# Optimization experiments

Hardware: AMD Instinct MI355X
Metric: run time of the kernel (lower is better)

The kernel has to match this reference:

```python
import jax, jax.numpy as jnp
import numpy as np

N = 50000        # nodes
E = 800000       # edges
F_IN = 128       # dataset.num_features (== dim*heads so all conv layers share in_channels)
DIM = 32         # mParams['dim']
HEADS = 4        # mParams['num_heads']
HC = DIM * HEADS # 128
DEPTH = 2        # mParams['c_depth'] -> total conv layers = DEPTH + 1 = 3
L = DEPTH + 1
DIM2 = 16        # ceil(DIM/2)
NCLS = 6
SLOPE = 0.2      # GATv2Conv default negative_slope


def setup_inputs() -> dict:
    key = jax.random.key(0)
    ks = jax.random.split(key, 20)
    def lin(k, fan_in, shape):
        return jax.random.normal(k, shape, dtype=jnp.float32) / np.sqrt(fan_in)
    x = jax.random.normal(ks[0], (N, F_IN), dtype=jnp.float32)
    edge_index = jax.random.randint(ks[1], (2, E), 0, N, dtype=jnp.int64)
    batch = jnp.zeros((N,), dtype=jnp.int64)
    # stacked GATv2Conv params (all layers have in_channels = 128)
    Wl = lin(ks[2], F_IN, (L, F_IN, HC))   # lin_l weight (source transform)
    Wr = lin(ks[3], F_IN, (L, F_IN, HC))   # lin_r weight (target transform)
    bl = jnp.zeros((L, HC), dtype=jnp.float32)
    br = jnp.zeros((L, HC), dtype=jnp.float32)
    att = lin(ks[4], DIM, (L, HEADS, DIM)) # attention vector a
    cb = jnp.zeros((L, HC), dtype=jnp.float32)  # conv output bias
    W1 = lin(ks[5], HC, (HC, DIM));   b1 = jnp.zeros((DIM,), jnp.float32)
    W2 = lin(ks[6], DIM, (DIM, DIM2)); b2 = jnp.zeros((DIM2,), jnp.float32)
    W3 = lin(ks[7], 2 * DIM2, (2 * DIM2, NCLS)); b3 = jnp.zeros((NCLS,), jnp.float32)
    return {"x": x, "edge_index": edge_index, "batch": batch,
            "Wl": Wl, "Wr": Wr, "bl": bl, "br": br, "att": att, "cb": cb,
            "W1": W1, "b1": b1, "W2": W2, "b2": b2, "W3": W3, "b3": b3}


def _gatv2_layer(h, src, dst, Wl, Wr, bl, br, att, cb):
    # h: [N, F]; src/dst: [Ea] (self-loops included)
    xl = (h @ Wl + bl).reshape(N, HEADS, DIM)  # source-side transform
    xr = (h @ Wr + br).reshape(N, HEADS, DIM)  # target-side transform
    msg = xl[src] + xr[dst]                    # [Ea, H, C]
    e = jnp.where(msg > 0, msg, SLOPE * msg)   # leaky_relu
    score = jnp.einsum('ehc,hc->eh', e, att)   # [Ea, H]
    # scatter-softmax over destination nodes
    m = jax.ops.segment_max(score, dst, num_segments=N)        # [N, H]
    ex = jnp.exp(score - m[dst])
    s = jax.ops.segment_sum(ex, dst, num_segments=N)           # [N, H]
    alpha = ex / (s[dst] + 1e-16)                              # [Ea, H]
    out = jax.ops.segment_sum(alpha[:, :, None] * xl[src], dst, num_segments=N)
    return out.reshape(N, HC) + cb


def reference(x, edge_index, batch, Wl, Wr, bl, br, att, cb, W1, b1, W2, b2, W3, b3):
    src0, dst0 = edge_index[0], edge_index[1]
    loop = jnp.arange(N, dtype=edge_index.dtype)
    src = jnp.concatenate([src0, loop])  # GATv2Conv add_self_loops=True
    dst = jnp.concatenate([dst0, loop])
    h = x
    for i in range(L):
        h = jax.nn.relu(_gatv2_layer(h, src, dst, Wl[i], Wr[i], bl[i], br[i], att[i], cb[i]))
    h = jax.nn.relu(h @ W1 + b1)
    h = jax.nn.relu(h @ W2 + b2)
    # dropout(p=0.5) is identity in eval mode
    e = jnp.concatenate([h[src0], h[dst0]], axis=1)  # [E, 2*DIM2]
    out = e @ W3 + b3                                # [E, NCLS]
    return (out, e)
```

## Files before the change

kernel.cpp:

```cpp
#include <hip/hip_runtime.h>
#include <hip/hip_bf16.h>

typedef __hip_bfloat16 bf16;
typedef __attribute__((ext_vector_type(8))) short bf16x8;
typedef __attribute__((ext_vector_type(4))) float f32x4;

#define N_NODES 50000
#define E_EDGES 800000
#define EA (E_EDGES + N_NODES)
#define HC 128
#define HEADS 4
#define DIM 32
#define DIM2 16
#define NCLS 6
#define SLOPE 0.2f
#define XN (N_NODES * HC)
#define GM 32
#define HSTRIDE 152
#define WSWZ_L 32768
#define SCHUNK 49

#define P_CVTI (2 * E_EDGES)
#define P_PRM  6390
#define P_WSWZ (3 * WSWZ_L)
#define P_TOT  (P_CVTI + P_PRM + P_WSWZ)

__device__ __forceinline__ float b2f(bf16 v) { return __bfloat162float(v); }
__device__ __forceinline__ unsigned short f2bfu(float f) {
    bf16 b = __float2bfloat16(f);
    return *(unsigned short*)&b;
}
__device__ __forceinline__ unsigned packbf(float a, float b) {
    return (unsigned)f2bfu(a) | ((unsigned)f2bfu(b) << 16);
}

__device__ __forceinline__ void block_detect(const void* wptr, const void* eptr,
                                             int* det, int& isf32, int& is64) {
    int tid = threadIdx.x;
    if (tid == 0) { det[0] = 0; det[1] = 0; }
    __syncthreads();
    const unsigned short* w = (const unsigned short*)wptr;
    int badf = 0;
    for (int i = tid; i < 1024; i += 256) {
        unsigned v = w[i];
        unsigned ex = (v >> 7) & 0xFF;
        if (v != 0 && (ex < 90 || ex > 150)) badf++;
    }
    const int* ei = (const int*)eptr;
    int nz = 0;
    for (int i = tid; i < 1024; i += 256) {
        if (ei[2 * i + 1] != 0) nz++;
    }
    if (badf) atomicAdd(&det[0], badf);
    if (nz)   atomicAdd(&det[1], nz);
    __syncthreads();
    isf32 = det[0] > 100;
    is64  = det[1] < 100;
}

__global__ __launch_bounds__(256) void k_prep(
        const void* eraw, const void* sWl, const void* sWr,
        const void* sbl, const void* sbr, const void* satt, const void* scb,
        const void* sW1, const void* sb1, const void* sW2, const void* sb2,
        const void* sW3, const void* sb3,
        int* __restrict__ eidx, int* __restrict__ off,
        float* __restrict__ prm, unsigned short* __restrict__ wswz) {
    __shared__ int det[2];
    int isf32, is64;
    block_detect(sWl, eraw, det, isf32, is64);

    int i = blockIdx.x * 256 + threadIdx.x;
    if (i < P_CVTI) {
        int v = is64 ? (int)((const long long*)eraw)[i] : ((const int*)eraw)[i];
        if (v < 0) v = 0;
        if (v >= N_NODES) v = N_NODES - 1;
        eidx[i] = v;
        if (i >= E_EDGES) atomicAdd(&off[v], 1);
        return;
    }
    i -= P_CVTI;
    if (i < P_PRM) {
        int j = i + 98304;
        const void* src; float* dst; int o;
        if      (j < 98688)  { src = sbl;  dst = prm + 98304;  o = j - 98304; }
        else if (j < 99072)  { src = sbr;  dst = prm + 98688;  o = j - 98688; }
        else if (j < 99456)  { src = satt; dst = prm + 99072;  o = j - 99072; }
        else if (j < 99840)  { src = scb;  dst = prm + 99456;  o = j - 99456; }
        else if (j < 103936) { src = sW1;  dst = prm + 99840;  o = j - 99840; }
        else if (j < 103968) { src = sb1;  dst = prm + 103936; o = j - 103936; }
        else if (j < 104480) { src = sW2;  dst = prm + 103968; o = j - 103968; }
        else if (j < 104496) { src = sb2;  dst = prm + 104480; o = j - 104480; }
        else if (j < 104688) { src = sW3;  dst = prm + 104496; o = j - 104496; }
        else                 { src = sb3;  dst = prm + 104688; o = j - 104688; }
        dst[o] = isf32 ? ((const float*)src)[o] : b2f(((const bf16*)src)[o]);
        return;
    }
    i -= P_PRM;
    if (i >= P_WSWZ) return;
    int L = i / WSWZ_L;
    int e = i % WSWZ_L;
    int ntile = e >> 11;
    int r2 = e & 2047;
    int ks = r2 >> 9;
    int r3 = r2 & 511;
    int lane = r3 >> 3;
    int j = r3 & 7;
    int col = ntile * 16 + (lane & 15);
    int k = ks * 32 + (lane >> 4) * 8 + j;
    const void* src = (col < HC) ? sWl : sWr;
    int idx = L * HC * HC + k * HC + (col & (HC - 1));
    float v = isf32 ? ((const float*)src)[idx] : b2f(((const bf16*)src)[idx]);
    wswz[i] = f2bfu(v);
}

__global__ __launch_bounds__(1024) void k_scan(int* __restrict__ off) {
    __shared__ int s[1024];
    int tid = threadIdx.x;
    int base = tid * SCHUNK;
    int sum = 0;
    for (int k = 0; k < SCHUNK; k++) {
        int idx = base + k;
        if (idx < N_NODES) sum += off[idx] + 1;
    }
    s[tid] = sum;
    __syncthreads();
    for (int o = 1; o < 1024; o <<= 1) {
        int t = (tid >= o) ? s[tid - o] : 0;
        __syncthreads();
        s[tid] += t;
        __syncthreads();
    }
    int run = (tid == 0) ? 0 : s[tid - 1];
    for (int k = 0; k < SCHUNK; k++) {
        int idx = base + k;
        if (idx < N_NODES) {
            int c = off[idx] + 1;
            off[idx] = run;
            run += c;
        }
    }
    if (tid == 0) off[N_NODES] = EA;
}

__global__ void k_scatter(const int* __restrict__ eidx, const int* __restrict__ off,
                          int* __restrict__ fill, int* __restrict__ csrsrc) {
    int e = blockIdx.x * blockDim.x + threadIdx.x;
    if (e >= EA) return;
    int src, dst;
    if (e < E_EDGES) { src = eidx[e]; dst = eidx[E_EDGES + e]; }
    else             { src = dst = e - E_EDGES; }
    int pos = off[dst] + atomicAdd(&fill[dst], 1);
    if (pos >= 0 && pos < EA) csrsrc[pos] = src;
}

__global__ __launch_bounds__(256) void k_gemm_mfma(
        const void* __restrict__ hsrc, const void* wdet, const void* edet,
        int detect_in,
        const unsigned short* __restrict__ wswz,
        const float* __restrict__ bl, const float* __restrict__ br,
        unsigned* __restrict__ xlbf, float* __restrict__ xr) {
    __shared__ unsigned short hs[GM * HSTRIDE];
    __shared__ int det[2];
    int tid = threadIdx.x;
    int wave = tid >> 6, lane = tid & 63;
    long row0 = (long)blockIdx.x * GM;

    int f32in = 0;
    if (detect_in) {
        int is64d;
        block_detect(wdet, edet, det, f32in, is64d);
    }

    if (f32in) {
        for (int idx = tid; idx < GM * 64; idx += 256) {
            int r = idx >> 6, cp = idx & 63;
            float v0 = 0.f, v1 = 0.f;
            if (row0 + r < N_NODES) {
                const float2 hv = ((const float2*)((const float*)hsrc + (row0 + r) * HC))[cp];
                v0 = hv.x; v1 = hv.y;
            }
            *(unsigned*)&hs[r * HSTRIDE + cp * 2] = packbf(v0, v1);
        }
    } else {
        for (int idx = tid; idx < GM * 64; idx += 256) {
            int r = idx >> 6, cp = idx & 63;
            unsigned u = 0;
            if (row0 + r < N_NODES)
                u = ((const unsigned*)hsrc)[(row0 + r) * (HC / 2) + cp];
            *(unsigned*)&hs[r * HSTRIDE + cp * 2] = u;
        }
    }
    __syncthreads();

    int q = lane >> 4, l16 = lane & 15;
    for (int nt = 0; nt < 4; nt++) {
        int colbase = wave * 64 + nt * 16;
        int col = colbase + l16;
        int ntile = colbase >> 4;
        f32x4 acc0 = {0.f, 0.f, 0.f, 0.f};
        f32x4 acc1 = {0.f, 0.f, 0.f, 0.f};
#pragma unroll
        for (int ks = 0; ks < 4; ks++) {
            bf16x8 bfrag = *(const bf16x8*)(wswz + (((ntile * 4 + ks) * 64 + lane) << 3));
            bf16x8 a0 = *(const bf16x8*)(hs + l16 * HSTRIDE + ks * 32 + q * 8);
            bf16x8 a1 = *(const bf16x8*)(hs + (16 + l16) * HSTRIDE + ks * 32 + q * 8);
            acc0 = __builtin_amdgcn_mfma_f32_16x16x32_bf16(a0, bfrag, acc0, 0, 0, 0);
            acc1 = __builtin_amdgcn_mfma_f32_16x16x32_bf16(a1, bfrag, acc1, 0, 0, 0);
        }
        if (col < HC) {
            float bias = bl[col];
#pragma unroll
            for (int reg = 0; reg < 4; reg++) {
                float v0 = acc0[reg] + bias;
                float v1 = acc1[reg] + bias;
                float p0 = __shfl_xor(v0, 1);
                float p1 = __shfl_xor(v1, 1);
                if ((lane & 1) == 0) {
                    long n0 = row0 + q * 4 + reg;
                    long n1 = row0 + 16 + q * 4 + reg;
                    unsigned u0 = packbf(v0, p0);
                    unsigned u1 = packbf(v1, p1);
                    int cp = col >> 1;
                    if (n0 < N_NODES) xlbf[n0 * (HC / 2) + cp] = u0;
                    if (n1 < N_NODES) xlbf[n1 * (HC / 2) + cp] = u1;
                }
            }
        } else {
            int c = col - HC;
            float bias = br[c];
#pragma unroll
            for (int reg = 0; reg < 4; reg++) {
                long n0 = row0 + q * 4 + reg;
                long n1 = row0 + 16 + q * 4 + reg;
                if (n0 < N_NODES) xr[n0 * HC + c] = acc0[reg] + bias;
                if (n1 < N_NODES) xr[n1 * HC + c] = acc1[reg] + bias;
            }
        }
    }
}

__global__ __launch_bounds__(256) void k_attn(
        const unsigned* __restrict__ xlbf, const float* __restrict__ xr,
        const int* __restrict__ off, const int* __restrict__ csrsrc,
        const float* __restrict__ att, const float* __restrict__ cb,
        void* __restrict__ hout, int out_bf16) {
    int wave = threadIdx.x >> 6;
    int lane = threadIdx.x & 63;
    int node = blockIdx.x * 4 + wave;
    if (node >= N_NODES) return;
    int grp = lane >> 4;
    int gl  = lane & 15;
    int fb  = gl * 8;
    int head = fb >> 5;

    const float4* xrp = (const float4*)(xr + (long)node * HC + fb);
    float4 xa = xrp[0], xb = xrp[1];
    const float4* ap = (const float4*)(att + head * DIM + (fb & 31));
    float4 aa = ap[0], ab = ap[1];

    int e0 = off[node], e1 = off[node + 1];
    if (e0 < 0) e0 = 0;
    if (e1 > EA) e1 = EA;
    if (e1 <= e0) {
        if (grp == 0) {
            if (out_bf16) {
                uint4 z = {0u, 0u, 0u, 0u};
                *(uint4*)((unsigned*)hout + (long)node * (HC / 2) + gl * 4) = z;
            } else {
                float4 z = make_float4(0.f, 0.f, 0.f, 0.f);
                ((float4*)((float*)hout + (long)node * HC + fb))[0] = z;
                ((float4*)((float*)hout + (long)node * HC + fb))[1] = z;
            }
        }
        return;
    }
    int klast = e1 - 1;

    int k0 = e0 + grp;
    int ka = k0 < klast ? k0 : klast;
    int kb = (k0 + 4) < klast ? (k0 + 4) : klast;
    int sa = csrsrc[ka];
    int sb = csrsrc[kb];
    uint4 u0 = ((const uint4*)(xlbf + (long)sa * (HC / 2)))[gl];
    uint4 u1 = ((const uint4*)(xlbf + (long)sb * (HC / 2)))[gl];

    float m = -1e30f, ssum = 0.f;
    float acc[8];
#pragma unroll
    for (int j = 0; j < 8; j++) acc[j] = 0.f;

    for (int kk = k0; kk < e1; kk += 4) {
        uint4 cur = u0;
        u0 = u1;
        int kp = (kk + 8) < klast ? (kk + 8) : klast;
        int sp = csrsrc[kp];
        u1 = ((const uint4*)(xlbf + (long)sp * (HC / 2)))[gl];

        float x0 = __uint_as_float(cur.x << 16);
        float x1 = __uint_as_float(cur.x & 0xffff0000u);
        float x2 = __uint_as_float(cur.y << 16);
        float x3 = __uint_as_float(cur.y & 0xffff0000u);
        float x4 = __uint_as_float(cur.z << 16);
        float x5 = __uint_as_float(cur.z & 0xffff0000u);
        float x6 = __uint_as_float(cur.w << 16);
        float x7 = __uint_as_float(cur.w & 0xffff0000u);
        float m0 = x0 + xa.x, m1 = x1 + xa.y, m2 = x2 + xa.z, m3 = x3 + xa.w;
        float m4 = x4 + xb.x, m5 = x5 + xb.y, m6 = x6 + xb.z, m7 = x7 + xb.w;
        float l0 = fmaxf(m0, SLOPE * m0), l1 = fmaxf(m1, SLOPE * m1);
        float l2 = fmaxf(m2, SLOPE * m2), l3 = fmaxf(m3, SLOPE * m3);
        float l4 = fmaxf(m4, SLOPE * m4), l5 = fmaxf(m5, SLOPE * m5);
        float l6 = fmaxf(m6, SLOPE * m6), l7 = fmaxf(m7, SLOPE * m7);
        float p = l0 * aa.x + l1 * aa.y + l2 * aa.z + l3 * aa.w
                + l4 * ab.x + l5 * ab.y + l6 * ab.z + l7 * ab.w;
        p += __shfl_xor(p, 1);
        p += __shfl_xor(p, 2);
        float mn = fmaxf(m, p);
        float sc = __expf(m - mn);
        float ex = __expf(p - mn);
        ssum = ssum * sc + ex;
        acc[0] = acc[0] * sc + ex * x0;
        acc[1] = acc[1] * sc + ex * x1;
        acc[2] = acc[2] * sc + ex * x2;
        acc[3] = acc[3] * sc + ex * x3;
        acc[4] = acc[4] * sc + ex * x4;
        acc[5] = acc[5] * sc + ex * x5;
        acc[6] = acc[6] * sc + ex * x6;
        acc[7] = acc[7] * sc + ex * x7;
        m = mn;
    }

#pragma unroll
    for (int d = 16; d <= 32; d <<= 1) {
        float mo = __shfl_xor(m, d);
        float so = __shfl_xor(ssum, d);
        float ao[8];
#pragma unroll
        for (int j = 0; j < 8; j++) ao[j] = __shfl_xor(acc[j], d);
        float mn = fmaxf(m, mo);
        float s1 = __expf(m - mn);
        float s2 = __expf(mo - mn);
        ssum = ssum * s1 + so * s2;
#pragma unroll
        for (int j = 0; j < 8; j++) acc[j] = acc[j] * s1 + ao[j] * s2;
        m = mn;
    }

    if (grp == 0) {
        float inv = 1.f / (ssum + 1e-16f);
        const float4* cbp = (const float4*)(cb + fb);
        float4 c0 = cbp[0], c1 = cbp[1];
        float o0 = fmaxf(acc[0] * inv + c0.x, 0.f);
        float o1 = fmaxf(acc[1] * inv + c0.y, 0.f);
        float o2 = fmaxf(acc[2] * inv + c0.z, 0.f);
        float o3 = fmaxf(acc[3] * inv + c0.w, 0.f);
        float o4 = fmaxf(acc[4] * inv + c1.x, 0.f);
        float o5 = fmaxf(acc[5] * inv + c1.y, 0.f);
        float o6 = fmaxf(acc[6] * inv + c1.z, 0.f);
        float o7 = fmaxf(acc[7] * inv + c1.w, 0.f);
        if (out_bf16) {
            uint4 w;
            w.x = packbf(o0, o1);
            w.y = packbf(o2, o3);
            w.z = packbf(o4, o5);
            w.w = packbf(o6, o7);
            *(uint4*)((unsigned*)hout + (long)node * (HC / 2) + gl * 4) = w;
        } else {
            float4 a0 = make_float4(o0, o1, o2, o3);
            float4 a1 = make_float4(o4, o5, o6, o7);
            float4* op = (float4*)((float*)hout + (long)node * HC + fb);
            op[0] = a0;
            op[1] = a1;
        }
    }
}

__global__ __launch_bounds__(256) void k_mlp(
        const float* __restrict__ h, const float* __restrict__ W1,
        const float* __restrict__ b1, const float* __restrict__ W2,
        const float* __restrict__ b2, float* __restrict__ h3) {
    __shared__ float w1s[HC * DIM];
    __shared__ float hs[16 * HC];
    __shared__ float h2s[16 * DIM];
    __shared__ float w2s[DIM * DIM2];
    int tid = threadIdx.x;
    long row0 = (long)blockIdx.x * 16;
    for (int idx = tid; idx < HC * DIM; idx += 256) w1s[idx] = W1[idx];
    for (int idx = tid; idx < DIM * DIM2; idx += 256) w2s[idx] = W2[idx];
    for (int idx = tid; idx < 16 * HC; idx += 256) {
        long g = row0 * HC + idx;
        hs[idx] = (g < (long)N_NODES * HC) ? h[g] : 0.f;
    }
    __syncthreads();
#pragma unroll
    for (int p = 0; p < 2; p++) {
        int idx = tid + p * 256;
        int r = idx >> 5, c = idx & 31;
        float acc = b1[c];
        for (int k = 0; k < HC; k++) acc += hs[r * HC + k] * w1s[k * DIM + c];
        h2s[r * DIM + c] = acc > 0.f ? acc : 0.f;
    }
    __syncthreads();
    int r = tid >> 4, c = tid & 15;
    float acc = b2[c];
    for (int k = 0; k < DIM; k++) acc += h2s[r * DIM + k] * w2s[k * DIM2 + c];
    long row = row0 + r;
    if (row < N_NODES) h3[row * DIM2 + c] = acc > 0.f ? acc : 0.f;
}

__global__ __launch_bounds__(256) void k_out(
        const float* __restrict__ h3, const int* __restrict__ eidx,
        const float* __restrict__ W3, const float* __restrict__ b3,
        void* __restrict__ dout, const void* wdet, const void* edet) {
    __shared__ float w3s[2 * DIM2 * NCLS];
    __shared__ float bs[NCLS];
    __shared__ int det[2];
    int isf32, is64d;
    block_detect(wdet, edet, det, isf32, is64d);
    int tid = threadIdx.x;
    if (tid < 2 * DIM2 * NCLS) w3s[tid] = W3[tid];
    if (tid < NCLS) bs[tid] = b3[tid];
    __syncthreads();
    int e = blockIdx.x * 256 + tid;
    if (e >= E_EDGES) return;
    int src = eidx[e], dst = eidx[E_EDGES + e];
    float v[2 * DIM2];
    const float4* ps = (const float4*)(h3 + (long)src * DIM2);
    const float4* pd = (const float4*)(h3 + (long)dst * DIM2);
#pragma unroll
    for (int q = 0; q < 4; q++) {
        float4 t = ps[q];
        v[q * 4 + 0] = t.x; v[q * 4 + 1] = t.y; v[q * 4 + 2] = t.z; v[q * 4 + 3] = t.w;
    }
#pragma unroll
    for (int q = 0; q < 4; q++) {
        float4 t = pd[q];
        v[16 + q * 4 + 0] = t.x; v[16 + q * 4 + 1] = t.y; v[16 + q * 4 + 2] = t.z; v[16 + q * 4 + 3] = t.w;
    }
    float o[NCLS];
#pragma unroll
    for (int j = 0; j < NCLS; j++) {
        float acc = bs[j];
#pragma unroll
        for (int k = 0; k < 2 * DIM2; k++) acc += v[k] * w3s[k * NCLS + j];
        o[j] = acc;
    }
    if (isf32) {
        float* out0 = (float*)dout;
#pragma unroll
        for (int j = 0; j < NCLS; j++) out0[(long)e * NCLS + j] = o[j];
        float4* eo = (float4*)((float*)dout + (long)E_EDGES * NCLS) + (long)e * 8;
#pragma unroll
        for (int q = 0; q < 8; q++)
            eo[q] = make_float4(v[q * 4], v[q * 4 + 1], v[q * 4 + 2], v[q * 4 + 3]);
    } else {
        bf16* out0 = (bf16*)dout;
#pragma unroll
        for (int j = 0; j < NCLS; j++) out0[(long)e * NCLS + j] = __float2bfloat16(o[j]);
        uint4* eo = (uint4*)((bf16*)dout + (long)E_EDGES * NCLS) + (long)e * 4;
#pragma unroll
        for (int q = 0; q < 4; q++) {
            uint4 w;
            w.x = packbf(v[q * 8 + 0], v[q * 8 + 1]);
            w.y = packbf(v[q * 8 + 2], v[q * 8 + 3]);
            w.z = packbf(v[q * 8 + 4], v[q * 8 + 5]);
            w.w = packbf(v[q * 8 + 6], v[q * 8 + 7]);
            eo[q] = w;
        }
    }
}

extern "C" void kernel_launch(void* const* d_in, const int* in_sizes, int n_in,
                              void* d_out, int out_size, void* d_ws, size_t ws_size,
                              hipStream_t stream) {
    float* wsf   = (float*)d_ws;
    float* h     = wsf + 16;
    float* xl    = h  + (long)N_NODES * HC;
    float* xr    = xl + (long)N_NODES * HC;
    float* prm   = xr + (long)N_NODES * HC;
    unsigned short* wswz = (unsigned short*)(prm + 110000);
    int*   eidx  = (int*)(wswz + P_WSWZ);
    int*   off   = eidx + 2 * E_EDGES;
    int*   fill  = off + (N_NODES + 1);
    int*   csr   = fill + N_NODES;
    unsigned* xlbf = (unsigned*)xl;
    float* h3 = xl;

    float* pbl = prm + 98304;
    float* pbr = prm + 98688;
    float* patt= prm + 99072;
    float* pcb = prm + 99456;
    float* pW1 = prm + 99840;
    float* pb1 = prm + 103936;
    float* pW2 = prm + 103968;
    float* pb2 = prm + 104480;
    float* pW3 = prm + 104496;
    float* pb3 = prm + 104688;

    hipMemsetAsync(off, 0, (size_t)(2 * N_NODES + 1) * sizeof(int), stream);

    k_prep<<<(P_TOT + 255) / 256, 256, 0, stream>>>(
        d_in[1], d_in[3], d_in[4], d_in[5], d_in[6], d_in[7], d_in[8],
        d_in[9], d_in[10], d_in[11], d_in[12], d_in[13], d_in[14],
        eidx, off, prm, wswz);

    k_scan<<<1, 1024, 0, stream>>>(off);
    k_scatter<<<(EA + 255) / 256, 256, 0, stream>>>(eidx, off, fill, csr);

    for (int i = 0; i < 3; i++) {
        k_gemm_mfma<<<(N_NODES + GM - 1) / GM, 256, 0, stream>>>(
            i == 0 ? (const void*)d_in[0] : (const void*)h,
            d_in[3], d_in[1], i == 0 ? 1 : 0,
            wswz + (long)i * WSWZ_L, pbl + (long)i * HC, pbr + (long)i * HC,
            xlbf, xr);
        k_attn<<<(N_NODES + 3) / 4, 256, 0, stream>>>(
            xlbf, xr, off, csr, patt + (long)i * HEADS * DIM, pcb + (long)i * HC,
            (void*)h, i < 2 ? 1 : 0);
    }

    k_mlp<<<(N_NODES + 15) / 16, 256, 0, stream>>>(h, pW1, pb1, pW2, pb2, h3);

    k_out<<<(E_EDGES + 255) / 256, 256, 0, stream>>>(h3, eidx, pW3, pb3, d_out,
                                                     d_in[3], d_in[1]);
}
```

Measured before the change: 657.4 us.

## Replace single-block degree scan with three-pass multi-block scan

The exclusive prefix sum over node degrees used to run in one 1024-thread block, each thread walking a strided chunk of 49 entries. It now runs as three kernels: a per-block scan over 49 blocks, a one-wave scan of the block totals, and an add-back pass. This spreads the serial scan across the GPU, with coalesced access, at the cost of two extra kernel launches and a small partials buffer placed after the CSR array in the workspace.

```diff
diff --git a/kernel.cpp b/kernel.cpp
--- a/kernel.cpp
+++ b/kernel.cpp
@@ -18,7 +18,7 @@
 #define GM 32
 #define HSTRIDE 152
 #define WSWZ_L 32768
-#define SCHUNK 49
+#define NCHUNK ((N_NODES + 1023) / 1024)
 
 #define P_CVTI (2 * E_EDGES)
 #define P_PRM  6390
@@ -113,16 +113,12 @@
     wswz[i] = f2bfu(v);
 }
 
-__global__ __launch_bounds__(1024) void k_scan(int* __restrict__ off) {
+__global__ __launch_bounds__(1024) void k_scan1(int* __restrict__ off, int* __restrict__ part) {
     __shared__ int s[1024];
     int tid = threadIdx.x;
-    int base = tid * SCHUNK;
-    int sum = 0;
-    for (int k = 0; k < SCHUNK; k++) {
-        int idx = base + k;
-        if (idx < N_NODES) sum += off[idx] + 1;
-    }
-    s[tid] = sum;
+    int i = blockIdx.x * 1024 + tid;
+    int v = (i < N_NODES) ? off[i] + 1 : 0;
+    s[tid] = v;
     __syncthreads();
     for (int o = 1; o < 1024; o <<= 1) {
         int t = (tid >= o) ? s[tid - o] : 0;
@@ -130,16 +126,25 @@
         s[tid] += t;
         __syncthreads();
     }
-    int run = (tid == 0) ? 0 : s[tid - 1];
-    for (int k = 0; k < SCHUNK; k++) {
-        int idx = base + k;
-        if (idx < N_NODES) {
-            int c = off[idx] + 1;
-            off[idx] = run;
-            run += c;
-        }
-    }
-    if (tid == 0) off[N_NODES] = EA;
+    if (i < N_NODES) off[i] = s[tid] - v;
+    if (tid == 1023) part[blockIdx.x] = s[1023];
+}
+
+__global__ __launch_bounds__(64) void k_scan2(int* __restrict__ part) {
+    int tid = threadIdx.x;
+    int v = (tid < NCHUNK) ? part[tid] : 0;
+    int orig = v;
+    for (int o = 1; o < 64; o <<= 1) {
+        int t = __shfl_up(v, o);
+        if (tid >= o) v += t;
+    }
+    if (tid < NCHUNK) part[tid] = v - orig;
+}
+
+__global__ __launch_bounds__(1024) void k_scan3(int* __restrict__ off, const int* __restrict__ part) {
+    int i = blockIdx.x * 1024 + threadIdx.x;
+    if (i < N_NODES) off[i] += part[blockIdx.x];
+    if (i == 0) off[N_NODES] = EA;
 }
 
 __global__ void k_scatter(const int* __restrict__ eidx, const int* __restrict__ off,
@@ -482,6 +487,7 @@
     int*   off   = eidx + 2 * E_EDGES;
     int*   fill  = off + (N_NODES + 1);
     int*   csr   = fill + N_NODES;
+    int*   part  = csr + EA;
     unsigned* xlbf = (unsigned*)xl;
     float* h3 = xl;
 
@@ -503,7 +509,9 @@
         d_in[9], d_in[10], d_in[11], d_in[12], d_in[13], d_in[14],
         eidx, off, prm, wswz);
 
-    k_scan<<<1, 1024, 0, stream>>>(off);
+    k_scan1<<<NCHUNK, 1024, 0, stream>>>(off, part);
+    k_scan2<<<1, 64, 0, stream>>>(part);
+    k_scan3<<<NCHUNK, 1024, 0, stream>>>(off, part);
     k_scatter<<<(EA + 255) / 256, 256, 0, stream>>>(eidx, off, fill, csr);
 
     for (int i = 0; i < 3; i++) {
```

Result: faster. 574.8 us (-12.6%).
